# Kernel optimization log

Hardware: AMD Instinct MI355X
Metric: run time of the kernel (lower is better)

Reference implementation:

```python
import jax, jax.numpy as jnp
import numpy as np

F = 16384   # n_features
D = 768     # d_model
B = 2       # batch
S = 256     # seq len
C = 16      # connections per downstream feature
M = F * C   # total connections


def setup_inputs() -> dict:
    key = jax.random.key(0)
    k1, k2, k3, k4 = jax.random.split(key, 4)
    up_facts = jax.random.normal(k1, (B, S, F), dtype=jnp.float32)
    down_encoder = jax.random.normal(k2, (F, D), dtype=jnp.float32) * 0.02
    up_decoder = jax.random.normal(k3, (D, F), dtype=jnp.float32) * 0.02
    # connection_mask.nonzero() is row-major: i sorted, C targets per row
    i_indices = jnp.repeat(jnp.arange(F, dtype=jnp.int32), C)  # [M]
    j_indices = jax.random.randint(k4, (M,), 0, F, dtype=jnp.int32)  # [M]
    return {
        "up_facts": up_facts,
        "down_encoder": down_encoder,
        "up_decoder": up_decoder,
        "i_indices": i_indices,
        "j_indices": j_indices,
    }


def reference(up_facts, down_encoder, up_decoder, i_indices, j_indices):
    # up_facts: [B,S,F]; down_encoder: [F,D]; up_decoder: [D,F]
    b, s, f = up_facts.shape
    m = i_indices.shape[0]
    # per-connection virtual weight: values[m] = down_encoder[i[m]] . up_decoder[:, j[m]]
    values = jnp.einsum("md,dm->m", down_encoder[i_indices], up_decoder[:, j_indices])  # [M]
    # gather upstream feature activations and scale
    scaled = up_facts[:, :, j_indices] * values[None, None, :]  # [B,S,M]
    # scatter_add over last axis into downstream feature bins (i is constant across B,S)
    flat = scaled.reshape(b * s, m).T  # [M, B*S]
    contrib = jax.ops.segment_sum(flat, i_indices, num_segments=f)  # [F, B*S]
    return contrib.T.reshape(b, s, f)
```

## Files before the change

kernel.cpp:

```cpp
#include <hip/hip_runtime.h>
#include <hip/hip_bf16.h>

#define F_ 16384
#define D_ 768
#define C_ 16
#define BS_ 512
#define M_ (F_*C_)

static __device__ __forceinline__ float bf2f(unsigned short u) {
    return __uint_as_float(((unsigned int)u) << 16);
}
static __device__ __forceinline__ unsigned short f2bf(float f) {
    return __bfloat16_as_ushort(__float2bfloat16(f));
}

__global__ __launch_bounds__(256) void k_transpose_bf16(const float* __restrict__ in,
                                                        unsigned short* __restrict__ out) {
    __shared__ float tile[64][65];
    int c4 = threadIdx.x & 15;
    int r  = threadIdx.x >> 4;
    int fbase = blockIdx.x * 64;
    int dbase = blockIdx.y * 64;
#pragma unroll
    for (int k = 0; k < 4; ++k) {
        int drow = r + k * 16;
        float4 v = *(const float4*)(in + (size_t)(dbase + drow) * F_ + fbase + c4 * 4);
        tile[drow][c4 * 4 + 0] = v.x;
        tile[drow][c4 * 4 + 1] = v.y;
        tile[drow][c4 * 4 + 2] = v.z;
        tile[drow][c4 * 4 + 3] = v.w;
    }
    __syncthreads();
    int dp = threadIdx.x & 15;
    int fr = threadIdx.x >> 4;
#pragma unroll
    for (int k = 0; k < 4; ++k) {
        int frow = fr + k * 16;
        float v0 = tile[4 * dp + 0][frow];
        float v1 = tile[4 * dp + 1][frow];
        float v2 = tile[4 * dp + 2][frow];
        float v3 = tile[4 * dp + 3][frow];
        uint2 p;
        p.x = ((unsigned int)f2bf(v1) << 16) | (unsigned int)f2bf(v0);
        p.y = ((unsigned int)f2bf(v3) << 16) | (unsigned int)f2bf(v2);
        *(uint2*)(out + (size_t)(fbase + frow) * D_ + dbase + dp * 4) = p;
    }
}

__global__ __launch_bounds__(256) void k_values(const float* __restrict__ enc,
                                                const unsigned short* __restrict__ decT,
                                                const int* __restrict__ jidx,
                                                unsigned int* __restrict__ packed) {
    int f = blockIdx.x;
    int lane = threadIdx.x & 63;
    int wave = threadIdx.x >> 6;
    const float4* erow = (const float4*)(enc + (size_t)f * D_);
    float4 e[3];
    e[0] = erow[lane];
    e[1] = erow[lane + 64];
    e[2] = erow[lane + 128];
    int4 j4 = *(const int4*)(jidx + (f << 4) + (wave << 2));
    int js[4] = {j4.x, j4.y, j4.z, j4.w};
    ushort4 g[4][3];
#pragma unroll
    for (int t = 0; t < 4; ++t) {
        const ushort4* drow = (const ushort4*)(decT + (size_t)js[t] * D_);
        g[t][0] = drow[lane];
        g[t][1] = drow[lane + 64];
        g[t][2] = drow[lane + 128];
    }
#pragma unroll
    for (int t = 0; t < 4; ++t) {
        float acc = 0.f;
#pragma unroll
        for (int k = 0; k < 3; ++k) {
            float4 ev = e[k];
            ushort4 dv = g[t][k];
            acc += ev.x * bf2f(dv.x) + ev.y * bf2f(dv.y)
                 + ev.z * bf2f(dv.z) + ev.w * bf2f(dv.w);
        }
#pragma unroll
        for (int off = 32; off > 0; off >>= 1)
            acc += __shfl_down(acc, off, 64);
        if (lane == 0)
            packed[(f << 4) + (wave << 2) + t] =
                ((unsigned int)f2bf(acc) << 16) | (unsigned int)js[t];
    }
}

__global__ __launch_bounds__(512) void k_out(const float* __restrict__ up,
                                             const unsigned int* __restrict__ packed,
                                             float* __restrict__ out) {
    __shared__ unsigned int rowp[F_];
    int bs0  = (blockIdx.x >> 1) << 1;
    int half = blockIdx.x & 1;
    const float4* u0 = (const float4*)(up + (size_t)bs0 * F_);
    const float4* u1 = (const float4*)(up + (size_t)(bs0 + 1) * F_);
#pragma unroll
    for (int k = 0; k < 8; ++k) {
        int idx = threadIdx.x + k * 512;
        float4 a = u0[idx];
        float4 b = u1[idx];
        uint4 p;
        p.x = ((unsigned int)f2bf(b.x) << 16) | (unsigned int)f2bf(a.x);
        p.y = ((unsigned int)f2bf(b.y) << 16) | (unsigned int)f2bf(a.y);
        p.z = ((unsigned int)f2bf(b.z) << 16) | (unsigned int)f2bf(a.z);
        p.w = ((unsigned int)f2bf(b.w) << 16) | (unsigned int)f2bf(a.w);
        ((uint4*)rowp)[idx] = p;
    }
    __syncthreads();
    int f0 = half << 13;
#pragma unroll 4
    for (int it = 0; it < 16; ++it) {
        int f = f0 + threadIdx.x + it * 512;
        const uint4* sp = (const uint4*)(packed + ((size_t)f << 4));
        float a0 = 0.f, a1 = 0.f;
#pragma unroll
        for (int q = 0; q < 4; ++q) {
            uint4 w = sp[q];
#define CONN(ww) { unsigned int p_ = rowp[(ww) & 0xffffu];                  \
                   float v_ = __uint_as_float((ww) & 0xffff0000u);          \
                   a0 += __uint_as_float(p_ << 16) * v_;                    \
                   a1 += __uint_as_float(p_ & 0xffff0000u) * v_; }
            CONN(w.x) CONN(w.y) CONN(w.z) CONN(w.w)
#undef CONN
        }
        out[(size_t)bs0 * F_ + f] = a0;
        out[(size_t)(bs0 + 1) * F_ + f] = a1;
    }
}

extern "C" void kernel_launch(void* const* d_in, const int* in_sizes, int n_in,
                              void* d_out, int out_size, void* d_ws, size_t ws_size,
                              hipStream_t stream) {
    const float* up   = (const float*)d_in[0];
    const float* enc  = (const float*)d_in[1];
    const float* dec  = (const float*)d_in[2];
    const int*   jidx = (const int*)d_in[4];
    float*       out  = (float*)d_out;

    size_t decT_bytes = (size_t)F_ * D_ * sizeof(unsigned short);
    unsigned short* decT   = (unsigned short*)d_ws;
    unsigned int*   packed = (unsigned int*)((char*)d_ws + decT_bytes);

    k_transpose_bf16<<<dim3(F_ / 64, D_ / 64), 256, 0, stream>>>(dec, decT);
    k_values<<<F_, 256, 0, stream>>>(enc, decT, jidx, packed);
    k_out<<<BS_, 512, 0, stream>>>(up, packed, out);
}
```

Baseline: 222.9 us.

## Process 16 features per block in k_values with double-buffered gathers

k_values now has each block handle 16 downstream features instead of one. The block stages their j indices in shared memory and software-pipelines the encoder-row loads and decoder-row gathers with two register buffers, so the loads for the next feature overlap the dot-product compute of the current one. The aim is to hide gather latency and cut per-block launch overhead. The cost is higher register pressure from the doubled buffers and far fewer blocks (1024), which may lower occupancy.

```diff
diff --git a/kernel.cpp b/kernel.cpp
--- a/kernel.cpp
+++ b/kernel.cpp
@@ -6,6 +6,7 @@
 #define C_ 16
 #define BS_ 512
 #define M_ (F_*C_)
+#define FPB_ 16
 
 static __device__ __forceinline__ float bf2f(unsigned short u) {
     return __uint_as_float(((unsigned int)u) << 16);
@@ -47,34 +48,38 @@
     }
 }
 
-__global__ __launch_bounds__(256) void k_values(const float* __restrict__ enc,
-                                                const unsigned short* __restrict__ decT,
-                                                const int* __restrict__ jidx,
-                                                unsigned int* __restrict__ packed) {
-    int f = blockIdx.x;
-    int lane = threadIdx.x & 63;
-    int wave = threadIdx.x >> 6;
-    const float4* erow = (const float4*)(enc + (size_t)f * D_);
-    float4 e[3];
+static __device__ __forceinline__ void v_load_e(const float* __restrict__ enc,
+                                                int fc, int lane, float4 e[3]) {
+    const float4* erow = (const float4*)(enc + (size_t)fc * D_);
     e[0] = erow[lane];
     e[1] = erow[lane + 64];
     e[2] = erow[lane + 128];
-    int4 j4 = *(const int4*)(jidx + (f << 4) + (wave << 2));
-    int js[4] = {j4.x, j4.y, j4.z, j4.w};
-    ushort4 g[4][3];
+}
+
+static __device__ __forceinline__ void v_gather(const unsigned short* __restrict__ decT,
+                                                const int* jsh, int ff, int wave,
+                                                int lane, int js[4], ushort4 g[4][3]) {
 #pragma unroll
     for (int t = 0; t < 4; ++t) {
-        const ushort4* drow = (const ushort4*)(decT + (size_t)js[t] * D_);
+        int j = jsh[(ff << 4) + (wave << 2) + t];
+        js[t] = j;
+        const ushort4* drow = (const ushort4*)(decT + (size_t)j * D_);
         g[t][0] = drow[lane];
         g[t][1] = drow[lane + 64];
         g[t][2] = drow[lane + 128];
     }
+}
+
+static __device__ __forceinline__ void v_compute(unsigned int* __restrict__ packed,
+                                                 int fc, int wave, int lane,
+                                                 const float4 e[3], const int js[4],
+                                                 const ushort4 g[4][3]) {
 #pragma unroll
     for (int t = 0; t < 4; ++t) {
         float acc = 0.f;
 #pragma unroll
         for (int k = 0; k < 3; ++k) {
-            float4 ev = e[k];
+            float4  ev = e[k];
             ushort4 dv = g[t][k];
             acc += ev.x * bf2f(dv.x) + ev.y * bf2f(dv.y)
                  + ev.z * bf2f(dv.z) + ev.w * bf2f(dv.w);
@@ -83,8 +88,40 @@
         for (int off = 32; off > 0; off >>= 1)
             acc += __shfl_down(acc, off, 64);
         if (lane == 0)
-            packed[(f << 4) + (wave << 2) + t] =
+            packed[(fc << 4) + (wave << 2) + t] =
                 ((unsigned int)f2bf(acc) << 16) | (unsigned int)js[t];
+    }
+}
+
+__global__ __launch_bounds__(256) void k_values(const float* __restrict__ enc,
+                                                const unsigned short* __restrict__ decT,
+                                                const int* __restrict__ jidx,
+                                                unsigned int* __restrict__ packed) {
+    const int lane = threadIdx.x & 63;
+    const int wave = threadIdx.x >> 6;
+    const int f0 = blockIdx.x * FPB_;
+
+    __shared__ int jsh[FPB_ * C_];
+    jsh[threadIdx.x] = jidx[(f0 << 4) + threadIdx.x];
+    __syncthreads();
+
+    float4  eA[3], eB[3];
+    int     jA[4], jB[4];
+    ushort4 gA[4][3], gB[4][3];
+
+    v_load_e(enc, f0, lane, eA);
+    v_gather(decT, jsh, 0, wave, lane, jA, gA);
+
+#pragma unroll
+    for (int p = 0; p < FPB_ / 2; ++p) {
+        v_load_e(enc, f0 + 2 * p + 1, lane, eB);
+        v_gather(decT, jsh, 2 * p + 1, wave, lane, jB, gB);
+        v_compute(packed, f0 + 2 * p, wave, lane, eA, jA, gA);
+        if (p < FPB_ / 2 - 1) {
+            v_load_e(enc, f0 + 2 * p + 2, lane, eA);
+            v_gather(decT, jsh, 2 * p + 2, wave, lane, jA, gA);
+        }
+        v_compute(packed, f0 + 2 * p + 1, wave, lane, eB, jB, gB);
     }
 }
 
@@ -144,6 +181,6 @@
     unsigned int*   packed = (unsigned int*)((char*)d_ws + decT_bytes);
 
     k_transpose_bf16<<<dim3(F_ / 64, D_ / 64), 256, 0, stream>>>(dec, decT);
-    k_values<<<F_, 256, 0, stream>>>(enc, decT, jidx, packed);
+    k_values<<<F_ / FPB_, 256, 0, stream>>>(enc, decT, jidx, packed);
     k_out<<<BS_, 512, 0, stream>>>(up, packed, out);
 }
```

After: 226.8 us. Within noise of the previous version (+1.7%).

## Quantize decoder and encoder to int8 with block scales and use sdot4

Applied to the files above, without the earlier changes.

The transposed decoder copy is now stored as int8 with one scale per 64-element block instead of bf16. The encoder row is quantized to int8 on the fly, with a scale per 64-element group. The per-connection dot products use the packed int8 dot instruction. This halves the bytes of the random gathered decoder rows and the transpose writes, at the cost of extra max-reduction and quantization work and lower numerical accuracy.

```diff
diff --git a/kernel.cpp b/kernel.cpp
--- a/kernel.cpp
+++ b/kernel.cpp
@@ -14,9 +14,24 @@
     return __bfloat16_as_ushort(__float2bfloat16(f));
 }
 
-__global__ __launch_bounds__(256) void k_transpose_bf16(const float* __restrict__ in,
-                                                        unsigned short* __restrict__ out) {
+#if __has_builtin(__builtin_amdgcn_sdot4)
+static __device__ __forceinline__ int sdot4(unsigned int a, unsigned int b, int c) {
+    return __builtin_amdgcn_sdot4((int)a, (int)b, c, false);
+}
+#else
+static __device__ __forceinline__ int sdot4(unsigned int a, unsigned int b, int c) {
+#pragma unroll
+    for (int i = 0; i < 4; ++i)
+        c += (int)(signed char)(a >> (8 * i)) * (int)(signed char)(b >> (8 * i));
+    return c;
+}
+#endif
+
+__global__ __launch_bounds__(256) void k_transpose_i8(const float* __restrict__ in,
+                                                      unsigned char* __restrict__ out,
+                                                      float* __restrict__ scales) {
     __shared__ float tile[64][65];
+    __shared__ float pmax[4][64];
     int c4 = threadIdx.x & 15;
     int r  = threadIdx.x >> 4;
     int fbase = blockIdx.x * 64;
@@ -31,24 +46,40 @@
         tile[drow][c4 * 4 + 3] = v.w;
     }
     __syncthreads();
+    {
+        int c = threadIdx.x & 63;
+        int q = threadIdx.x >> 6;
+        float m = 0.f;
+#pragma unroll
+        for (int i = 0; i < 16; ++i)
+            m = fmaxf(m, fabsf(tile[q * 16 + i][c]));
+        pmax[q][c] = m;
+    }
+    __syncthreads();
     int dp = threadIdx.x & 15;
     int fr = threadIdx.x >> 4;
 #pragma unroll
     for (int k = 0; k < 4; ++k) {
         int frow = fr + k * 16;
-        float v0 = tile[4 * dp + 0][frow];
-        float v1 = tile[4 * dp + 1][frow];
-        float v2 = tile[4 * dp + 2][frow];
-        float v3 = tile[4 * dp + 3][frow];
-        uint2 p;
-        p.x = ((unsigned int)f2bf(v1) << 16) | (unsigned int)f2bf(v0);
-        p.y = ((unsigned int)f2bf(v3) << 16) | (unsigned int)f2bf(v2);
-        *(uint2*)(out + (size_t)(fbase + frow) * D_ + dbase + dp * 4) = p;
+        float cmax = fmaxf(fmaxf(pmax[0][frow], pmax[1][frow]),
+                           fmaxf(pmax[2][frow], pmax[3][frow]));
+        float s  = cmax * (1.f / 127.f);
+        float rs = cmax > 0.f ? 127.f / cmax : 0.f;
+        int q0 = __float2int_rn(tile[4 * dp + 0][frow] * rs);
+        int q1 = __float2int_rn(tile[4 * dp + 1][frow] * rs);
+        int q2 = __float2int_rn(tile[4 * dp + 2][frow] * rs);
+        int q3 = __float2int_rn(tile[4 * dp + 3][frow] * rs);
+        unsigned int p = (q0 & 0xff) | ((q1 & 0xff) << 8)
+                       | ((q2 & 0xff) << 16) | ((q3 & 0xff) << 24);
+        *(unsigned int*)(out + (size_t)(fbase + frow) * D_ + dbase + dp * 4) = p;
+        if (dp == 0)
+            scales[((size_t)(fbase + frow) << 4) + (dbase >> 6)] = s;
     }
 }
 
 __global__ __launch_bounds__(256) void k_values(const float* __restrict__ enc,
-                                                const unsigned short* __restrict__ decT,
+                                                const unsigned char* __restrict__ dec8,
+                                                const float* __restrict__ scales,
                                                 const int* __restrict__ jidx,
                                                 unsigned int* __restrict__ packed) {
     int f = blockIdx.x;
@@ -61,23 +92,46 @@
     e[2] = erow[lane + 128];
     int4 j4 = *(const int4*)(jidx + (f << 4) + (wave << 2));
     int js[4] = {j4.x, j4.y, j4.z, j4.w};
-    ushort4 g[4][3];
+    unsigned int g[4][3];
+    float sd[4][3];
+    int sb = lane >> 4;
 #pragma unroll
     for (int t = 0; t < 4; ++t) {
-        const ushort4* drow = (const ushort4*)(decT + (size_t)js[t] * D_);
+        const unsigned int* drow = (const unsigned int*)(dec8 + (size_t)js[t] * D_);
         g[t][0] = drow[lane];
         g[t][1] = drow[lane + 64];
         g[t][2] = drow[lane + 128];
+        const float* srow = scales + ((size_t)js[t] << 4);
+        sd[t][0] = srow[sb];
+        sd[t][1] = srow[sb + 4];
+        sd[t][2] = srow[sb + 8];
+    }
+    unsigned int eq[3];
+    float se[3];
+#pragma unroll
+    for (int k = 0; k < 3; ++k) {
+        float4 v = e[k];
+        float m = fmaxf(fmaxf(fabsf(v.x), fabsf(v.y)),
+                        fmaxf(fabsf(v.z), fabsf(v.w)));
+#pragma unroll
+        for (int off = 1; off < 16; off <<= 1)
+            m = fmaxf(m, __shfl_xor(m, off, 64));
+        float rs = m > 0.f ? 127.f / m : 0.f;
+        se[k] = m * (1.f / 127.f);
+        int q0 = __float2int_rn(v.x * rs);
+        int q1 = __float2int_rn(v.y * rs);
+        int q2 = __float2int_rn(v.z * rs);
+        int q3 = __float2int_rn(v.w * rs);
+        eq[k] = (q0 & 0xff) | ((q1 & 0xff) << 8)
+              | ((q2 & 0xff) << 16) | ((q3 & 0xff) << 24);
     }
 #pragma unroll
     for (int t = 0; t < 4; ++t) {
         float acc = 0.f;
 #pragma unroll
         for (int k = 0; k < 3; ++k) {
-            float4 ev = e[k];
-            ushort4 dv = g[t][k];
-            acc += ev.x * bf2f(dv.x) + ev.y * bf2f(dv.y)
-                 + ev.z * bf2f(dv.z) + ev.w * bf2f(dv.w);
+            int d = sdot4(eq[k], g[t][k], 0);
+            acc = fmaf((float)d, se[k] * sd[t][k], acc);
         }
 #pragma unroll
         for (int off = 32; off > 0; off >>= 1)
@@ -139,11 +193,13 @@
     const int*   jidx = (const int*)d_in[4];
     float*       out  = (float*)d_out;
 
-    size_t decT_bytes = (size_t)F_ * D_ * sizeof(unsigned short);
-    unsigned short* decT   = (unsigned short*)d_ws;
-    unsigned int*   packed = (unsigned int*)((char*)d_ws + decT_bytes);
-
-    k_transpose_bf16<<<dim3(F_ / 64, D_ / 64), 256, 0, stream>>>(dec, decT);
-    k_values<<<F_, 256, 0, stream>>>(enc, decT, jidx, packed);
+    size_t dec8_bytes  = (size_t)F_ * D_;
+    size_t scale_bytes = (size_t)F_ * 16 * sizeof(float);
+    unsigned char* dec8   = (unsigned char*)d_ws;
+    float*         scales = (float*)((char*)d_ws + dec8_bytes);
+    unsigned int*  packed = (unsigned int*)((char*)d_ws + dec8_bytes + scale_bytes);
+
+    k_transpose_i8<<<dim3(F_ / 64, D_ / 64), 256, 0, stream>>>(dec, dec8, scales);
+    k_values<<<F_, 256, 0, stream>>>(enc, dec8, scales, jidx, packed);
     k_out<<<BS_, 512, 0, stream>>>(up, packed, out);
 }
```

Measured after the change: 205.8 us. 1.08x faster.
